# Performance work log

Measured on AMD Instinct MI355X. Metric: run time of the kernel, lower is better.

## Reference

```python
import jax, jax.numpy as jnp
import numpy as np

HEAD_DIM = 64
SCALE = 1.0 / np.sqrt(HEAD_DIM).astype(np.float32)


def setup_inputs() -> dict:
    key = jax.random.key(0)
    kq, kk, kv = jax.random.split(key, 3)
    shape = (2, 16, 2048, HEAD_DIM)  # [batch, num_heads, seq_len, head_dim]
    q = jax.random.normal(kq, shape, dtype=jnp.float32)
    k = jax.random.normal(kk, shape, dtype=jnp.float32)
    v = jax.random.normal(kv, shape, dtype=jnp.float32)
    # causal mask: True above the diagonal means 'masked' (no attention)
    mask = jnp.triu(jnp.ones((2048, 2048), dtype=bool), k=1)
    return {"q": q, "k": k, "v": v, "mask": mask}


def reference(q, k, v, mask):
    # scores: [b, h, s, s]
    scores = jnp.einsum("bhqd,bhkd->bhqk", q, k) * SCALE
    scores = jnp.where(mask[None, None, :, :], -jnp.inf, scores)
    attn_weights = jax.nn.softmax(scores, axis=-1)
    attn_weights = jnp.where(mask[None, None, :, :], 0.0, attn_weights)
    output = jnp.einsum("bhqk,bhkd->bhqd", attn_weights, v)
    return (output, attn_weights)
```

## Files before the change

### kernel.cpp

```cpp
#include <hip/hip_runtime.h>
#include <stdint.h>


#define SEQ 2048
#define HD  64

typedef __attribute__((ext_vector_type(8))) short short8;
typedef __attribute__((ext_vector_type(4))) float f32x4;

__device__ __forceinline__ short f2bf(float x) {
  uint32_t u = __builtin_bit_cast(uint32_t, x);
  u = (u + 0x7FFFu + ((u >> 16) & 1u)) >> 16;
  return (short)(uint16_t)u;
}
__device__ __forceinline__ float bf2f(short h) {
  uint32_t u = ((uint32_t)(uint16_t)h) << 16;
  return __builtin_bit_cast(float, u);
}
__device__ __forceinline__ int swz(int row, int col) {
  return (row << 6) + (col ^ ((row & 7) << 3));
}

#define MFMA16(a, b, c) __builtin_amdgcn_mfma_f32_16x16x32_bf16((a), (b), (c), 0, 0, 0)

__device__ __forceinline__ void cvt4(const f32x4 x, short8& h, short8& l, const int base) {
#pragma unroll
  for (int j = 0; j < 4; ++j) {
    const float fv = x[j];
    const short hb = f2bf(fv);
    h[base + j] = hb;
    l[base + j] = f2bf(fv - bf2f(hb));
  }
}

__device__ __forceinline__ void stage_K(const float* __restrict__ kp, int kt, int tid,
                                        short* lKh, short* lKl) {
  const int krow = tid >> 2;
  const int kd0  = (tid & 3) << 4;
  const f32x4* p4 = (const f32x4*)(kp + (size_t)((kt << 6) + krow) * HD + kd0);
  short8 h0, h1, l0, l1;
  cvt4(p4[0], h0, l0, 0);
  cvt4(p4[1], h0, l0, 4);
  cvt4(p4[2], h1, l1, 0);
  cvt4(p4[3], h1, l1, 4);
  *(short8*)&lKh[swz(krow, kd0)]     = h0;
  *(short8*)&lKh[swz(krow, kd0 + 8)] = h1;
  *(short8*)&lKl[swz(krow, kd0)]     = l0;
  *(short8*)&lKl[swz(krow, kd0 + 8)] = l1;
}

__device__ __forceinline__ void stage_V_t(const float* __restrict__ vp, int kt, int tid,
                                          short* lVh, short* lVl) {
  const int vrow = tid & 63;
  const int vd0  = (tid >> 6) << 4;
  const f32x4* p4 = (const f32x4*)(vp + (size_t)((kt << 6) + vrow) * HD + vd0);
#pragma unroll
  for (int g = 0; g < 4; ++g) {
    const f32x4 x = p4[g];
#pragma unroll
    for (int j = 0; j < 4; ++j) {
      const int dr = vd0 + g * 4 + j;
      const float fv = x[j];
      const short hb = f2bf(fv);
      lVh[swz(dr, vrow)] = hb;
      lVl[swz(dr, vrow)] = f2bf(fv - bf2f(hb));
    }
  }
}

__device__ __forceinline__ void qk_scores(const short* lKh, const short* lKl,
                                          const short8 qh[2], const short8 ql[2],
                                          int lg, int ln, f32x4 sc[4]) {
#pragma unroll
  for (int n = 0; n < 4; ++n) {
    f32x4 acc = {0.f, 0.f, 0.f, 0.f};
#pragma unroll
    for (int c = 0; c < 2; ++c) {
      const int bi = swz(n * 16 + ln, c * 32 + lg * 8);
      const short8 kh = *(const short8*)&lKh[bi];
      const short8 kl = *(const short8*)&lKl[bi];
      acc = MFMA16(qh[c], kh, acc);
      acc = MFMA16(ql[c], kh, acc);
      acc = MFMA16(qh[c], kl, acc);
    }
    sc[n] = acc;
  }
}

__global__ __launch_bounds__(256, 2) void attn_fwd(
    const float* __restrict__ gq, const float* __restrict__ gk,
    const float* __restrict__ gv, float* __restrict__ go,
    float* __restrict__ ga) {
  __shared__ __align__(16) short lKh[64 * 64];
  __shared__ __align__(16) short lKl[64 * 64];
  __shared__ __align__(16) short lVh[64 * 64];
  __shared__ __align__(16) short lVl[64 * 64];
  __shared__ __align__(16) short lPh[4][16 * 64];
  __shared__ __align__(16) short lPl[4][16 * 64];

  const int tid  = threadIdx.x;
  const int w    = tid >> 6;
  const int lane = tid & 63;
  const int lg   = lane >> 4;
  const int ln   = lane & 15;

  const int qb = 31 - (int)(blockIdx.x & 31);
  const int bh = blockIdx.x >> 5;

  const float* qp = gq + (size_t)bh * SEQ * HD;
  const float* kp = gk + (size_t)bh * SEQ * HD;
  const float* vp = gv + (size_t)bh * SEQ * HD;
  float* op = go + (size_t)bh * SEQ * HD;
  float* ap = ga + (size_t)bh * SEQ * SEQ;

  const int qbase  = qb << 6;
  const int wqbase = qbase + (w << 4);

  short8 qh[2], ql[2];
  {
    const float* qrow = qp + (size_t)(wqbase + ln) * HD;
#pragma unroll
    for (int c = 0; c < 2; ++c) {
      const int d0 = c * 32 + lg * 8;
      const f32x4 x0 = *(const f32x4*)(qrow + d0);
      const f32x4 x1 = *(const f32x4*)(qrow + d0 + 4);
#pragma unroll
      for (int j = 0; j < 4; ++j) {
        float xs = x0[j] * 0.125f;
        short hb = f2bf(xs);
        qh[c][j] = hb;
        ql[c][j] = f2bf(xs - bf2f(hb));
        xs = x1[j] * 0.125f;
        hb = f2bf(xs);
        qh[c][4 + j] = hb;
        ql[c][4 + j] = f2bf(xs - bf2f(hb));
      }
    }
  }

  f32x4 oacc[4];
  const f32x4 Z4 = {0.f, 0.f, 0.f, 0.f};
#pragma unroll
  for (int n = 0; n < 4; ++n) oacc[n] = Z4;
  float lpart[4] = {0.f, 0.f, 0.f, 0.f};

  for (int kt = 0; kt <= qb; ++kt) {
    __syncthreads();
    stage_K(kp, kt, tid, lKh, lKl);
    stage_V_t(vp, kt, tid, lVh, lVl);
    __syncthreads();

    f32x4 sc[4];
    qk_scores(lKh, lKl, qh, ql, lg, ln, sc);

#pragma unroll
    for (int n = 0; n < 4; ++n) {
      const int kg = (kt << 6) + n * 16 + ln;
#pragma unroll
      for (int r = 0; r < 4; ++r) {
        const int qg = wqbase + lg * 4 + r;
        const float e = (kg <= qg) ? __expf(sc[n][r]) : 0.f;
        lpart[r] += e;
        const short eh = f2bf(e);
        const short el = f2bf(e - bf2f(eh));
        const int pi = swz(lg * 4 + r, n * 16 + ln);
        lPh[w][pi] = eh;
        lPl[w][pi] = el;
      }
    }
    __syncthreads();

#pragma unroll
    for (int c = 0; c < 2; ++c) {
      const int ac = swz(ln, c * 32 + lg * 8);
      const short8 ph = *(const short8*)&lPh[w][ac];
      const short8 pl = *(const short8*)&lPl[w][ac];
#pragma unroll
      for (int n = 0; n < 4; ++n) {
        const int bi = swz(n * 16 + ln, c * 32 + lg * 8);
        const short8 vh = *(const short8*)&lVh[bi];
        const short8 vl = *(const short8*)&lVl[bi];
        oacc[n] = MFMA16(ph, vh, oacc[n]);
        oacc[n] = MFMA16(pl, vh, oacc[n]);
        oacc[n] = MFMA16(ph, vl, oacc[n]);
      }
    }
  }

  float linv[4];
#pragma unroll
  for (int r = 0; r < 4; ++r) {
    float s = lpart[r];
    s += __shfl_xor(s, 8, 64);
    s += __shfl_xor(s, 4, 64);
    s += __shfl_xor(s, 2, 64);
    s += __shfl_xor(s, 1, 64);
    linv[r] = 1.0f / s;
  }

#pragma unroll
  for (int n = 0; n < 4; ++n)
#pragma unroll
    for (int r = 0; r < 4; ++r)
      __builtin_nontemporal_store(oacc[n][r] * linv[r],
          &op[(size_t)(wqbase + lg * 4 + r) * HD + n * 16 + ln]);

  for (int kt = 0; kt <= qb; ++kt) {
    __syncthreads();
    stage_K(kp, kt, tid, lKh, lKl);
    __syncthreads();

    f32x4 sc[4];
    qk_scores(lKh, lKl, qh, ql, lg, ln, sc);

#pragma unroll
    for (int n = 0; n < 4; ++n) {
      const int kg = (kt << 6) + n * 16 + ln;
#pragma unroll
      for (int r = 0; r < 4; ++r) {
        const int qg = wqbase + lg * 4 + r;
        const float pv = (kg <= qg) ? __expf(sc[n][r]) * linv[r] : 0.f;
        __builtin_nontemporal_store(pv, &ap[(size_t)qg * SEQ + kg]);
      }
    }
  }

  const int zstart = (qb + 1) << 6;
  const int zc = SEQ - zstart;
  if (zc > 0) {
    for (int row = 0; row < 64; ++row) {
      float* dst = ap + (size_t)(qbase + row) * SEQ + zstart;
      for (int c = tid * 4; c < zc; c += 1024) {
        float* p = dst + c;
        __builtin_nontemporal_store(0.0f, p + 0);
        __builtin_nontemporal_store(0.0f, p + 1);
        __builtin_nontemporal_store(0.0f, p + 2);
        __builtin_nontemporal_store(0.0f, p + 3);
      }
    }
  }
}

extern "C" void kernel_launch(void* const* d_in, const int* in_sizes, int n_in,
                              void* d_out, int out_size, void* d_ws, size_t ws_size,
                              hipStream_t stream) {
  (void)in_sizes; (void)n_in; (void)out_size; (void)d_ws; (void)ws_size;
  const float* q = (const float*)d_in[0];
  const float* k = (const float*)d_in[1];
  const float* v = (const float*)d_in[2];
  float* o = (float*)d_out;
  float* a = o + (size_t)2 * 16 * SEQ * HD;
  attn_fwd<<<dim3(2 * 16 * (SEQ / 64)), dim3(256), 0, stream>>>(q, k, v, o, a);
}
```

Measured before the change: 856.1 us.

## Pre-split K/V to bf16 pairs, async LDS double-buffering, pair causal blocks

Adds two prep kernels that split K and the transposed V into swizzled bf16 hi/lo pairs in workspace. The attention kernel then stages tiles with global_load_lds into double-buffered shared memory, so the next tile's load overlaps the current tile's compute. Each block now processes two query blocks (31-z and z) so causal work is balanced across blocks. The cost is extra kernel launches and workspace traffic, plus fewer blocks (512), which may lower occupancy.

```diff
diff --git a/kernel.cpp b/kernel.cpp
--- a/kernel.cpp
+++ b/kernel.cpp
@@ -4,26 +4,33 @@
 
 #define SEQ 2048
 #define HD  64
+#define NBH 32
 
 typedef __attribute__((ext_vector_type(8))) short short8;
 typedef __attribute__((ext_vector_type(4))) float f32x4;
 
-__device__ __forceinline__ short f2bf(float x) {
+static __device__ __forceinline__ short f2bf(float x) {
   uint32_t u = __builtin_bit_cast(uint32_t, x);
   u = (u + 0x7FFFu + ((u >> 16) & 1u)) >> 16;
   return (short)(uint16_t)u;
 }
-__device__ __forceinline__ float bf2f(short h) {
+static __device__ __forceinline__ float bf2f(short h) {
   uint32_t u = ((uint32_t)(uint16_t)h) << 16;
   return __builtin_bit_cast(float, u);
 }
-__device__ __forceinline__ int swz(int row, int col) {
+static __device__ __forceinline__ int swz(int row, int col) {
   return (row << 6) + (col ^ ((row & 7) << 3));
 }
 
 #define MFMA16(a, b, c) __builtin_amdgcn_mfma_f32_16x16x32_bf16((a), (b), (c), 0, 0, 0)
 
-__device__ __forceinline__ void cvt4(const f32x4 x, short8& h, short8& l, const int base) {
+#define GLOAD16(gsrc, ldst)                                             \
+  __builtin_amdgcn_global_load_lds(                                     \
+      (const __attribute__((address_space(1))) void*)(gsrc),            \
+      (__attribute__((address_space(3))) void*)(ldst), 16, 0, 0)
+
+static __device__ __forceinline__ void cvt4(const f32x4 x, short8& h, short8& l,
+                                            const int base) {
 #pragma unroll
   for (int j = 0; j < 4; ++j) {
     const float fv = x[j];
@@ -33,70 +40,60 @@
   }
 }
 
-__device__ __forceinline__ void stage_K(const float* __restrict__ kp, int kt, int tid,
-                                        short* lKh, short* lKl) {
-  const int krow = tid >> 2;
-  const int kd0  = (tid & 3) << 4;
-  const f32x4* p4 = (const f32x4*)(kp + (size_t)((kt << 6) + krow) * HD + kd0);
-  short8 h0, h1, l0, l1;
-  cvt4(p4[0], h0, l0, 0);
-  cvt4(p4[1], h0, l0, 4);
-  cvt4(p4[2], h1, l1, 0);
-  cvt4(p4[3], h1, l1, 4);
-  *(short8*)&lKh[swz(krow, kd0)]     = h0;
-  *(short8*)&lKh[swz(krow, kd0 + 8)] = h1;
-  *(short8*)&lKl[swz(krow, kd0)]     = l0;
-  *(short8*)&lKl[swz(krow, kd0 + 8)] = l1;
-}
-
-__device__ __forceinline__ void stage_V_t(const float* __restrict__ vp, int kt, int tid,
-                                          short* lVh, short* lVl) {
-  const int vrow = tid & 63;
-  const int vd0  = (tid >> 6) << 4;
-  const f32x4* p4 = (const f32x4*)(vp + (size_t)((kt << 6) + vrow) * HD + vd0);
-#pragma unroll
-  for (int g = 0; g < 4; ++g) {
-    const f32x4 x = p4[g];
+__global__ void prep_k(const float* __restrict__ K, short* __restrict__ Kh,
+                       short* __restrict__ Kl) {
+  const int gidx = blockIdx.x * 256 + threadIdx.x;
+  const int row = gidx >> 3, g = gidx & 7;
+  const f32x4* s = (const f32x4*)(K + (size_t)row * HD + g * 8);
+  short8 h, l;
+  cvt4(s[0], h, l, 0);
+  cvt4(s[1], h, l, 4);
+  const size_t di = (size_t)row * HD + ((g ^ (row & 7)) << 3);
+  *(short8*)&Kh[di] = h;
+  *(short8*)&Kl[di] = l;
+}
+
+__global__ void prep_v(const float* __restrict__ V, short* __restrict__ Vh,
+                       short* __restrict__ Vl) {
+  __shared__ float t[64][65];
+  const int bh = blockIdx.x >> 5, kt = blockIdx.x & 31;
+  const float* src = V + ((size_t)bh * SEQ + kt * 64) * HD;
+#pragma unroll
+  for (int i = 0; i < 4; ++i) {
+    const int ch = threadIdx.x + i * 256;
+    const int r = ch >> 4, c4 = (ch & 15) << 2;
+    const f32x4 x = *(const f32x4*)(src + r * HD + c4);
+#pragma unroll
+    for (int j = 0; j < 4; ++j) t[r][c4 + j] = x[j];
+  }
+  __syncthreads();
+#pragma unroll
+  for (int i = 0; i < 2; ++i) {
+    const int oid = threadIdx.x + i * 256;
+    const int d = oid >> 3, g = oid & 7;
+    f32x4 a, b;
 #pragma unroll
     for (int j = 0; j < 4; ++j) {
-      const int dr = vd0 + g * 4 + j;
-      const float fv = x[j];
-      const short hb = f2bf(fv);
-      lVh[swz(dr, vrow)] = hb;
-      lVl[swz(dr, vrow)] = f2bf(fv - bf2f(hb));
-    }
+      a[j] = t[g * 8 + j][d];
+      b[j] = t[g * 8 + 4 + j][d];
+    }
+    short8 h, l;
+    cvt4(a, h, l, 0);
+    cvt4(b, h, l, 4);
+    const size_t di = ((size_t)bh * HD + d) * SEQ + kt * 64 + ((g ^ (d & 7)) << 3);
+    *(short8*)&Vh[di] = h;
+    *(short8*)&Vl[di] = l;
   }
 }
 
-__device__ __forceinline__ void qk_scores(const short* lKh, const short* lKl,
-                                          const short8 qh[2], const short8 ql[2],
-                                          int lg, int ln, f32x4 sc[4]) {
-#pragma unroll
-  for (int n = 0; n < 4; ++n) {
-    f32x4 acc = {0.f, 0.f, 0.f, 0.f};
-#pragma unroll
-    for (int c = 0; c < 2; ++c) {
-      const int bi = swz(n * 16 + ln, c * 32 + lg * 8);
-      const short8 kh = *(const short8*)&lKh[bi];
-      const short8 kl = *(const short8*)&lKl[bi];
-      acc = MFMA16(qh[c], kh, acc);
-      acc = MFMA16(ql[c], kh, acc);
-      acc = MFMA16(qh[c], kl, acc);
-    }
-    sc[n] = acc;
-  }
-}
-
 __global__ __launch_bounds__(256, 2) void attn_fwd(
-    const float* __restrict__ gq, const float* __restrict__ gk,
-    const float* __restrict__ gv, float* __restrict__ go,
-    float* __restrict__ ga) {
-  __shared__ __align__(16) short lKh[64 * 64];
-  __shared__ __align__(16) short lKl[64 * 64];
-  __shared__ __align__(16) short lVh[64 * 64];
-  __shared__ __align__(16) short lVl[64 * 64];
-  __shared__ __align__(16) short lPh[4][16 * 64];
-  __shared__ __align__(16) short lPl[4][16 * 64];
+    const float* __restrict__ gq,
+    const short* __restrict__ gKh, const short* __restrict__ gKl,
+    const short* __restrict__ gVh, const short* __restrict__ gVl,
+    float* __restrict__ go, float* __restrict__ ga) {
+  __shared__ __align__(16) short lK[2][2][4096];
+  __shared__ __align__(16) short lV[2][2][4096];
+  __shared__ __align__(16) short lP[2][4][1024];
 
   const int tid  = threadIdx.x;
   const int w    = tid >> 6;
@@ -104,138 +101,203 @@
   const int lg   = lane >> 4;
   const int ln   = lane & 15;
 
-  const int qb = 31 - (int)(blockIdx.x & 31);
-  const int bh = blockIdx.x >> 5;
-
-  const float* qp = gq + (size_t)bh * SEQ * HD;
-  const float* kp = gk + (size_t)bh * SEQ * HD;
-  const float* vp = gv + (size_t)bh * SEQ * HD;
+  const int bh = blockIdx.x >> 4;
+  const int z  = blockIdx.x & 15;
+
+  const float* qp  = gq  + (size_t)bh * SEQ * HD;
+  const short* Khb = gKh + (size_t)bh * SEQ * HD;
+  const short* Klb = gKl + (size_t)bh * SEQ * HD;
+  const short* Vhb = gVh + (size_t)bh * SEQ * HD;
+  const short* Vlb = gVl + (size_t)bh * SEQ * HD;
   float* op = go + (size_t)bh * SEQ * HD;
   float* ap = ga + (size_t)bh * SEQ * SEQ;
 
-  const int qbase  = qb << 6;
-  const int wqbase = qbase + (w << 4);
-
-  short8 qh[2], ql[2];
-  {
-    const float* qrow = qp + (size_t)(wqbase + ln) * HD;
-#pragma unroll
-    for (int c = 0; c < 2; ++c) {
-      const int d0 = c * 32 + lg * 8;
-      const f32x4 x0 = *(const f32x4*)(qrow + d0);
-      const f32x4 x1 = *(const f32x4*)(qrow + d0 + 4);
-#pragma unroll
-      for (int j = 0; j < 4; ++j) {
-        float xs = x0[j] * 0.125f;
-        short hb = f2bf(xs);
-        qh[c][j] = hb;
-        ql[c][j] = f2bf(xs - bf2f(hb));
-        xs = x1[j] * 0.125f;
-        hb = f2bf(xs);
-        qh[c][4 + j] = hb;
-        ql[c][4 + j] = f2bf(xs - bf2f(hb));
-      }
-    }
-  }
-
-  f32x4 oacc[4];
-  const f32x4 Z4 = {0.f, 0.f, 0.f, 0.f};
-#pragma unroll
-  for (int n = 0; n < 4; ++n) oacc[n] = Z4;
-  float lpart[4] = {0.f, 0.f, 0.f, 0.f};
-
-  for (int kt = 0; kt <= qb; ++kt) {
+  auto stage_k = [&](const short* th, const short* tl, short* bh_, short* bl_) {
+    const int o0 = w * 1024 + lane * 8;
+    GLOAD16(th + o0,       bh_ + w * 1024);
+    GLOAD16(th + o0 + 512, bh_ + w * 1024 + 512);
+    GLOAD16(tl + o0,       bl_ + w * 1024);
+    GLOAD16(tl + o0 + 512, bl_ + w * 1024 + 512);
+  };
+  auto stage_v = [&](const short* th, const short* tl, short* bh_, short* bl_) {
+    const int c0 = w * 128 + lane;
+    const int c1 = c0 + 64;
+    GLOAD16(th + (size_t)(c0 >> 3) * SEQ + (c0 & 7) * 8, bh_ + w * 1024);
+    GLOAD16(th + (size_t)(c1 >> 3) * SEQ + (c1 & 7) * 8, bh_ + w * 1024 + 512);
+    GLOAD16(tl + (size_t)(c0 >> 3) * SEQ + (c0 & 7) * 8, bl_ + w * 1024);
+    GLOAD16(tl + (size_t)(c1 >> 3) * SEQ + (c1 & 7) * 8, bl_ + w * 1024 + 512);
+  };
+
+  for (int sec = 0; sec < 2; ++sec) {
+    const int qb     = (sec == 0) ? (31 - z) : z;
+    const int qbase  = qb << 6;
+    const int wqbase = qbase + (w << 4);
+
+    short8 qh[2], ql[2];
+    {
+      const float* qrow = qp + (size_t)(wqbase + ln) * HD;
+#pragma unroll
+      for (int c = 0; c < 2; ++c) {
+        const int d0 = c * 32 + lg * 8;
+        const f32x4 x0 = *(const f32x4*)(qrow + d0);
+        const f32x4 x1 = *(const f32x4*)(qrow + d0 + 4);
+#pragma unroll
+        for (int j = 0; j < 4; ++j) {
+          float xs = x0[j] * 0.125f;
+          short hb = f2bf(xs);
+          qh[c][j] = hb;
+          ql[c][j] = f2bf(xs - bf2f(hb));
+          xs = x1[j] * 0.125f;
+          hb = f2bf(xs);
+          qh[c][4 + j] = hb;
+          ql[c][4 + j] = f2bf(xs - bf2f(hb));
+        }
+      }
+    }
+
+    f32x4 oacc[4];
+    const f32x4 Z4 = {0.f, 0.f, 0.f, 0.f};
+#pragma unroll
+    for (int n = 0; n < 4; ++n) oacc[n] = Z4;
+    float lpart[4] = {0.f, 0.f, 0.f, 0.f};
+
+    stage_k(Khb, Klb, lK[0][0], lK[0][1]);
+    stage_v(Vhb, Vlb, lV[0][0], lV[0][1]);
     __syncthreads();
-    stage_K(kp, kt, tid, lKh, lKl);
-    stage_V_t(vp, kt, tid, lVh, lVl);
+    int cur = 0;
+    for (int kt = 0; kt <= qb; ++kt, cur ^= 1) {
+      if (kt < qb) {
+        stage_k(Khb + (kt + 1) * 4096, Klb + (kt + 1) * 4096,
+                lK[cur ^ 1][0], lK[cur ^ 1][1]);
+        stage_v(Vhb + (kt + 1) * 64, Vlb + (kt + 1) * 64,
+                lV[cur ^ 1][0], lV[cur ^ 1][1]);
+      }
+      const short* bKh = lK[cur][0];
+      const short* bKl = lK[cur][1];
+      const short* bVh = lV[cur][0];
+      const short* bVl = lV[cur][1];
+
+      f32x4 sc[4];
+#pragma unroll
+      for (int n = 0; n < 4; ++n) {
+        f32x4 acc = Z4;
+#pragma unroll
+        for (int c = 0; c < 2; ++c) {
+          const int bi = swz(n * 16 + ln, c * 32 + lg * 8);
+          const short8 kh = *(const short8*)&bKh[bi];
+          const short8 kl = *(const short8*)&bKl[bi];
+          acc = MFMA16(qh[c], kh, acc);
+          acc = MFMA16(ql[c], kh, acc);
+          acc = MFMA16(qh[c], kl, acc);
+        }
+        sc[n] = acc;
+      }
+
+#pragma unroll
+      for (int n = 0; n < 4; ++n) {
+        const int kg = (kt << 6) + n * 16 + ln;
+#pragma unroll
+        for (int r = 0; r < 4; ++r) {
+          const int qg = wqbase + lg * 4 + r;
+          const float e = (kg <= qg) ? __expf(sc[n][r]) : 0.f;
+          lpart[r] += e;
+          const short eh = f2bf(e);
+          const short el = f2bf(e - bf2f(eh));
+          const int pi = swz(lg * 4 + r, n * 16 + ln);
+          lP[0][w][pi] = eh;
+          lP[1][w][pi] = el;
+        }
+      }
+      asm volatile("s_waitcnt lgkmcnt(0)" ::: "memory");
+      __builtin_amdgcn_sched_barrier(0);
+
+#pragma unroll
+      for (int c = 0; c < 2; ++c) {
+        const int ac = swz(ln, c * 32 + lg * 8);
+        const short8 ph = *(const short8*)&lP[0][w][ac];
+        const short8 pl = *(const short8*)&lP[1][w][ac];
+#pragma unroll
+        for (int n = 0; n < 4; ++n) {
+          const int bi = swz(n * 16 + ln, c * 32 + lg * 8);
+          const short8 vh = *(const short8*)&bVh[bi];
+          const short8 vl = *(const short8*)&bVl[bi];
+          oacc[n] = MFMA16(ph, vh, oacc[n]);
+          oacc[n] = MFMA16(pl, vh, oacc[n]);
+          oacc[n] = MFMA16(ph, vl, oacc[n]);
+        }
+      }
+      __syncthreads();
+    }
+
+    float linv[4];
+#pragma unroll
+    for (int r = 0; r < 4; ++r) {
+      float s = lpart[r];
+      s += __shfl_xor(s, 8, 64);
+      s += __shfl_xor(s, 4, 64);
+      s += __shfl_xor(s, 2, 64);
+      s += __shfl_xor(s, 1, 64);
+      linv[r] = 1.0f / s;
+    }
+
+#pragma unroll
+    for (int n = 0; n < 4; ++n)
+#pragma unroll
+      for (int r = 0; r < 4; ++r)
+        __builtin_nontemporal_store(oacc[n][r] * linv[r],
+            &op[(size_t)(wqbase + lg * 4 + r) * HD + n * 16 + ln]);
+
+    stage_k(Khb, Klb, lK[0][0], lK[0][1]);
     __syncthreads();
-
-    f32x4 sc[4];
-    qk_scores(lKh, lKl, qh, ql, lg, ln, sc);
-
-#pragma unroll
-    for (int n = 0; n < 4; ++n) {
-      const int kg = (kt << 6) + n * 16 + ln;
-#pragma unroll
-      for (int r = 0; r < 4; ++r) {
-        const int qg = wqbase + lg * 4 + r;
-        const float e = (kg <= qg) ? __expf(sc[n][r]) : 0.f;
-        lpart[r] += e;
-        const short eh = f2bf(e);
-        const short el = f2bf(e - bf2f(eh));
-        const int pi = swz(lg * 4 + r, n * 16 + ln);
-        lPh[w][pi] = eh;
-        lPl[w][pi] = el;
-      }
-    }
-    __syncthreads();
-
-#pragma unroll
-    for (int c = 0; c < 2; ++c) {
-      const int ac = swz(ln, c * 32 + lg * 8);
-      const short8 ph = *(const short8*)&lPh[w][ac];
-      const short8 pl = *(const short8*)&lPl[w][ac];
+    cur = 0;
+    for (int kt = 0; kt <= qb; ++kt, cur ^= 1) {
+      if (kt < qb)
+        stage_k(Khb + (kt + 1) * 4096, Klb + (kt + 1) * 4096,
+                lK[cur ^ 1][0], lK[cur ^ 1][1]);
+      const short* bKh = lK[cur][0];
+      const short* bKl = lK[cur][1];
+
+      f32x4 sc[4];
 #pragma unroll
       for (int n = 0; n < 4; ++n) {
-        const int bi = swz(n * 16 + ln, c * 32 + lg * 8);
-        const short8 vh = *(const short8*)&lVh[bi];
-        const short8 vl = *(const short8*)&lVl[bi];
-        oacc[n] = MFMA16(ph, vh, oacc[n]);
-        oacc[n] = MFMA16(pl, vh, oacc[n]);
-        oacc[n] = MFMA16(ph, vl, oacc[n]);
-      }
-    }
-  }
-
-  float linv[4];
-#pragma unroll
-  for (int r = 0; r < 4; ++r) {
-    float s = lpart[r];
-    s += __shfl_xor(s, 8, 64);
-    s += __shfl_xor(s, 4, 64);
-    s += __shfl_xor(s, 2, 64);
-    s += __shfl_xor(s, 1, 64);
-    linv[r] = 1.0f / s;
-  }
-
-#pragma unroll
-  for (int n = 0; n < 4; ++n)
-#pragma unroll
-    for (int r = 0; r < 4; ++r)
-      __builtin_nontemporal_store(oacc[n][r] * linv[r],
-          &op[(size_t)(wqbase + lg * 4 + r) * HD + n * 16 + ln]);
-
-  for (int kt = 0; kt <= qb; ++kt) {
-    __syncthreads();
-    stage_K(kp, kt, tid, lKh, lKl);
-    __syncthreads();
-
-    f32x4 sc[4];
-    qk_scores(lKh, lKl, qh, ql, lg, ln, sc);
-
-#pragma unroll
-    for (int n = 0; n < 4; ++n) {
-      const int kg = (kt << 6) + n * 16 + ln;
-#pragma unroll
-      for (int r = 0; r < 4; ++r) {
-        const int qg = wqbase + lg * 4 + r;
-        const float pv = (kg <= qg) ? __expf(sc[n][r]) * linv[r] : 0.f;
-        __builtin_nontemporal_store(pv, &ap[(size_t)qg * SEQ + kg]);
-      }
-    }
-  }
-
-  const int zstart = (qb + 1) << 6;
-  const int zc = SEQ - zstart;
-  if (zc > 0) {
-    for (int row = 0; row < 64; ++row) {
-      float* dst = ap + (size_t)(qbase + row) * SEQ + zstart;
-      for (int c = tid * 4; c < zc; c += 1024) {
-        float* p = dst + c;
-        __builtin_nontemporal_store(0.0f, p + 0);
-        __builtin_nontemporal_store(0.0f, p + 1);
-        __builtin_nontemporal_store(0.0f, p + 2);
-        __builtin_nontemporal_store(0.0f, p + 3);
+        f32x4 acc = Z4;
+#pragma unroll
+        for (int c = 0; c < 2; ++c) {
+          const int bi = swz(n * 16 + ln, c * 32 + lg * 8);
+          const short8 kh = *(const short8*)&bKh[bi];
+          const short8 kl = *(const short8*)&bKl[bi];
+          acc = MFMA16(qh[c], kh, acc);
+          acc = MFMA16(ql[c], kh, acc);
+          acc = MFMA16(qh[c], kl, acc);
+        }
+        sc[n] = acc;
+      }
+
+#pragma unroll
+      for (int n = 0; n < 4; ++n) {
+        const int kg = (kt << 6) + n * 16 + ln;
+#pragma unroll
+        for (int r = 0; r < 4; ++r) {
+          const int qg = wqbase + lg * 4 + r;
+          const float pv = (kg <= qg) ? __expf(sc[n][r]) * linv[r] : 0.f;
+          __builtin_nontemporal_store(pv, &ap[(size_t)qg * SEQ + kg]);
+        }
+      }
+      __syncthreads();
+    }
+
+    const int zstart = (qb + 1) << 6;
+    const int zc = SEQ - zstart;
+    if (zc > 0) {
+      for (int row = 0; row < 64; ++row) {
+        float* dst = ap + (size_t)(qbase + row) * SEQ + zstart;
+        for (int c = tid * 4; c < zc; c += 1024) {
+          float* p = dst + c;
+          __builtin_nontemporal_store(0.0f, p + 0);
+          __builtin_nontemporal_store(0.0f, p + 1);
+          __builtin_nontemporal_store(0.0f, p + 2);
+          __builtin_nontemporal_store(0.0f, p + 3);
+        }
       }
     }
   }
@@ -244,11 +306,19 @@
 extern "C" void kernel_launch(void* const* d_in, const int* in_sizes, int n_in,
                               void* d_out, int out_size, void* d_ws, size_t ws_size,
                               hipStream_t stream) {
-  (void)in_sizes; (void)n_in; (void)out_size; (void)d_ws; (void)ws_size;
+  (void)in_sizes; (void)n_in; (void)out_size; (void)ws_size;
   const float* q = (const float*)d_in[0];
   const float* k = (const float*)d_in[1];
   const float* v = (const float*)d_in[2];
   float* o = (float*)d_out;
-  float* a = o + (size_t)2 * 16 * SEQ * HD;
-  attn_fwd<<<dim3(2 * 16 * (SEQ / 64)), dim3(256), 0, stream>>>(q, k, v, o, a);
-}
+  float* a = o + (size_t)NBH * SEQ * HD;
+
+  short* Khi  = (short*)d_ws;
+  short* Klo  = Khi  + (size_t)NBH * SEQ * HD;
+  short* Vthi = Klo  + (size_t)NBH * SEQ * HD;
+  short* Vtlo = Vthi + (size_t)NBH * SEQ * HD;
+
+  prep_k<<<dim3(2048), dim3(256), 0, stream>>>(k, Khi, Klo);
+  prep_v<<<dim3(1024), dim3(256), 0, stream>>>(v, Vthi, Vtlo);
+  attn_fwd<<<dim3(512), dim3(256), 0, stream>>>(q, Khi, Klo, Vthi, Vtlo, o, a);
+}
```

Result: faster. 704.3 us (-17.7%).
